# Performance work log

Measured on AMD Instinct MI355X. Metric: run time of the kernel, lower is better.

The kernel has to match this reference:

```python
import jax, jax.numpy as jnp
import numpy as np
from jax import lax

B, H, W, C, NH = 16, 64, 64, 192, 6


def rope2d(x, h, w, c, base=10000.0):
    # 2D RoPE: channel_dims=(h,w), k_max = c // 4; angles (h,w,c//2)
    kmax = c // 4
    theta = 1.0 / (base ** (jnp.arange(kmax, dtype=jnp.float32) / kmax))
    ai = jnp.broadcast_to(jnp.arange(h, dtype=jnp.float32)[:, None, None] * theta, (h, w, kmax))
    aj = jnp.broadcast_to(jnp.arange(w, dtype=jnp.float32)[None, :, None] * theta, (h, w, kmax))
    ang = jnp.concatenate([ai, aj], axis=-1)  # (h,w,c//2)
    cos, sin = jnp.cos(ang), jnp.sin(ang)
    xr = x.reshape(*x.shape[:-1], c // 2, 2)
    xe, xo = xr[..., 0], xr[..., 1]
    # complex multiply (cos + i sin) * (xe + i xo)
    return jnp.stack([xe * cos - xo * sin, xe * sin + xo * cos], axis=-1).reshape(x.shape)


def setup_inputs() -> dict:
    key = jax.random.key(0)
    ks = jax.random.split(key, 4)
    return {
        "x": jax.random.normal(ks[0], (B, H, W, C), dtype=jnp.float32),
        "qk_w": jax.random.normal(ks[1], (2 * C, C), dtype=jnp.float32) * 0.02,
        "qk_b": jnp.zeros((2 * C,), dtype=jnp.float32),
        "lepe_w": jax.random.normal(ks[2], (C, 1, 3, 3), dtype=jnp.float32) * 0.1,
        "lepe_b": jnp.zeros((C,), dtype=jnp.float32),
    }


def reference(x, qk_w, qk_b, lepe_w, lepe_b):
    b, h, w, c = x.shape
    n = h * w
    nh = NH
    d = c // nh
    qk = x @ qk_w.T + qk_b  # (b,h,w,2c)
    q = jax.nn.elu(qk[..., :c]) + 1.0
    k = jax.nn.elu(qk[..., c:]) + 1.0
    q_rope = rope2d(q, h, w, c).reshape(b, n, nh, d).transpose(0, 2, 1, 3)  # (b,nh,n,d)
    k_rope = rope2d(k, h, w, c).reshape(b, n, nh, d).transpose(0, 2, 1, 3)
    qh = q.reshape(b, n, nh, d).transpose(0, 2, 1, 3)
    kh = k.reshape(b, n, nh, d).transpose(0, 2, 1, 3)
    vh = x.reshape(b, n, nh, d).transpose(0, 2, 1, 3)  # v = x
    kmean = kh.mean(axis=2)  # (b,nh,d)
    z = 1.0 / (jnp.einsum('bhnd,bhd->bhn', qh, kmean)[..., None] + 1e-6)  # (b,nh,n,1)
    scale = 1.0 / jnp.sqrt(jnp.float32(n))
    kv = jnp.einsum('bhnd,bhne->bhde', k_rope * scale, vh * scale)  # (b,nh,d,d)
    out = jnp.einsum('bhnd,bhde->bhne', q_rope, kv) * z  # (b,nh,n,d)
    out = out.transpose(0, 2, 1, 3).reshape(b, n, c)
    # LePE: depthwise 3x3 conv on v (= x) in NCHW
    v_nchw = x.transpose(0, 3, 1, 2)
    lepe = lax.conv_general_dilated(v_nchw, lepe_w, (1, 1), 'SAME',
                                    dimension_numbers=('NCHW', 'OIHW', 'NCHW'),
                                    feature_group_count=c)
    lepe = lepe + lepe_b[None, :, None, None]
    return out + lepe.transpose(0, 2, 3, 1).reshape(b, n, c)
```

## Files before the change

kernel.cpp:

```cpp
#include <hip/hip_runtime.h>
#include <hip/hip_bf16.h>

using short8  = __attribute__((ext_vector_type(8))) short;
using floatx4 = __attribute__((ext_vector_type(4))) float;

#define CC 192
#define CN 4096
#define NHEAD 6
#define DHEAD 32
#define NZERO (16 * NHEAD * DHEAD * DHEAD + 16 * NHEAD * DHEAD)
#define ZBLK ((NZERO + 255) / 256)
#define TBLK ((CN * 96 + 255) / 256)

__device__ __forceinline__ float bf2f(short s) {
    return __uint_as_float(((unsigned)(unsigned short)s) << 16);
}
__device__ __forceinline__ short f2bf(float f) {
    __hip_bfloat16 h = __float2bfloat16(f);
    return *(short*)&h;
}

__global__ void k0_all(float* __restrict__ zp, unsigned* __restrict__ tabp,
                       const float* __restrict__ qkw, __hip_bfloat16* __restrict__ wfr)
{
    int bid = blockIdx.x;
    if (bid < ZBLK) {
        int i = bid * 256 + threadIdx.x;
        if (i < NZERO) zp[i] = 0.f;
    } else if (bid < ZBLK + TBLK) {
        int idx = (bid - ZBLK) * 256 + threadIdx.x;
        if (idx >= CN * 96) return;
        int n = idx / 96, c2 = idx - n * 96;
        int h = n >> 6, w = n & 63;
        int i = (c2 < 48) ? c2 : c2 - 48;
        float pos = (float)((c2 < 48) ? h : w);
        float theta = expf(-(float)i * (9.210340371976184f / 48.0f));
        float ang = pos * theta;
        unsigned c = (unsigned)(unsigned short)f2bf(cosf(ang));
        unsigned s = (unsigned)(unsigned short)f2bf(sinf(ang));
        tabp[idx] = c | (s << 16);
    } else {
        int tid = (bid - ZBLK - TBLK) * 256 + threadIdx.x;
        if (tid >= 24 * 6 * 64) return;
        int lane = tid & 63;
        int ks = (tid >> 6) % 6;
        int nig = tid / (6 * 64);
        int col = nig * 16 + (lane & 15);
        int k = ks * 32 + (lane >> 4) * 8;
        const float4* src = (const float4*)(qkw + (long)col * CC + k);
        float4 f0 = src[0], f1 = src[1];
        short8 s;
        s[0] = f2bf(f0.x); s[1] = f2bf(f0.y); s[2] = f2bf(f0.z); s[3] = f2bf(f0.w);
        s[4] = f2bf(f1.x); s[5] = f2bf(f1.y); s[6] = f2bf(f1.z); s[7] = f2bf(f1.w);
        *(short8*)&wfr[(long)tid * 8] = s;
    }
}

__global__ __launch_bounds__(512)
void k1_gemm(const float* __restrict__ x, const __hip_bfloat16* __restrict__ wfr,
             const float* __restrict__ qkb,
             __hip_bfloat16* __restrict__ qws, __hip_bfloat16* __restrict__ kws,
             __hip_bfloat16* __restrict__ xbf)
{
    __shared__ __align__(16) short A_lds[128 * 200];
    __shared__ __align__(16) short B_lds[24 * 512];

    const int tid  = threadIdx.x;
    const int wid  = tid >> 6, lane = tid & 63;
    const int wm   = wid >> 1, wn = wid & 1;
    const int lrow = lane & 15;
    const int l4   = lane >> 4;
    const long rowBase = (long)blockIdx.x * 128;

#pragma unroll
    for (int it = 0; it < 6; ++it) {
        int slot = it * 512 + tid;
        int row = slot / 24, c0 = (slot - (slot / 24) * 24) * 8;
        const float4* src = (const float4*)(x + (rowBase + row) * CC + c0);
        float4 f0 = src[0], f1 = src[1];
        short8 s;
        s[0] = f2bf(f0.x); s[1] = f2bf(f0.y); s[2] = f2bf(f0.z); s[3] = f2bf(f0.w);
        s[4] = f2bf(f1.x); s[5] = f2bf(f1.y); s[6] = f2bf(f1.z); s[7] = f2bf(f1.w);
        *(short8*)&A_lds[row * 200 + c0] = s;
        *(short8*)&xbf[(rowBase + row) * CC + c0] = s;
    }

    floatx4 acc[2][12];
#pragma unroll
    for (int i = 0; i < 2; ++i)
#pragma unroll
        for (int j = 0; j < 12; ++j) acc[i][j] = (floatx4)0.f;

    for (int ks = 0; ks < 6; ++ks) {
        short8 bst[3];
#pragma unroll
        for (int j = 0; j < 3; ++j) {
            int s = j * 512 + tid;
            bst[j] = *(const short8*)&wfr[((long)((s >> 6) * 6 + ks) * 64 + (s & 63)) * 8];
        }
        __syncthreads();
#pragma unroll
        for (int j = 0; j < 3; ++j) {
            int s = j * 512 + tid;
            *(short8*)&B_lds[s * 8] = bst[j];
        }
        __syncthreads();

        short8 a0 = *(const short8*)&A_lds[(wm * 32 + lrow) * 200 + ks * 32 + l4 * 8];
        short8 a1 = *(const short8*)&A_lds[(wm * 32 + 16 + lrow) * 200 + ks * 32 + l4 * 8];
#pragma unroll
        for (int ni = 0; ni < 12; ++ni) {
            short8 bf = *(const short8*)&B_lds[(wn * 12 + ni) * 512 + lane * 8];
            acc[0][ni] = __builtin_amdgcn_mfma_f32_16x16x32_bf16(a0, bf, acc[0][ni], 0, 0, 0);
            acc[1][ni] = __builtin_amdgcn_mfma_f32_16x16x32_bf16(a1, bf, acc[1][ni], 0, 0, 0);
        }
    }

    __hip_bfloat16* dstbase = wn ? kws : qws;
#pragma unroll
    for (int ni = 0; ni < 12; ++ni) {
        int col_l = ni * 16 + lrow;
        float bias = qkb[wn * 192 + col_l];
#pragma unroll
        for (int mi = 0; mi < 2; ++mi) {
#pragma unroll
            for (int r = 0; r < 4; ++r) {
                int rowl = wm * 32 + mi * 16 + l4 * 4 + r;
                long rowg = rowBase + rowl;
                float v = acc[mi][ni][r] + bias;
                v = (v > 0.f) ? (v + 1.f) : expf(v);
                dstbase[rowg * CC + col_l] = __float2bfloat16(v);
            }
        }
    }
}

__global__ __launch_bounds__(256)
void k2_kv(const __hip_bfloat16* __restrict__ kws, const __hip_bfloat16* __restrict__ xbf,
           const unsigned* __restrict__ tabp, float* __restrict__ kv, float* __restrict__ kmean)
{
    int bid = blockIdx.x;
    int chunk = bid & 7;
    int hd = (bid >> 3) % NHEAD;
    int b = bid / (8 * NHEAD);
    int tid = threadIdx.x;
    int lane = tid & 63;

    __shared__ __align__(16) float S[9248];
    float* kr_s = S;
    float* v_s  = S + 4608;
    float* km_s = S + 9216;

    if (tid < 32) km_s[tid] = 0.f;

    const int krow = tid >> 2, kq = tid & 3;
    const int rq = tid >> 6, tile = tid & 63;
    const int dq = tile >> 3, eq = tile & 7;

    float acc[4][4];
#pragma unroll
    for (int i = 0; i < 4; ++i)
#pragma unroll
        for (int j = 0; j < 4; ++j) acc[i][j] = 0.f;
    float msum[8];
#pragma unroll
    for (int j = 0; j < 8; ++j) msum[j] = 0.f;

    const int n0 = chunk * 512;
    const long rb = (long)b * CN;

    short8 k8[2], v8[2];
    uint4  u[2];
#pragma unroll
    for (int p = 0; p < 2; ++p) {
        int n = n0 + p * 64 + krow;
        k8[p] = *(const short8*)&kws[(rb + n) * CC + hd * DHEAD + kq * 8];
        v8[p] = *(const short8*)&xbf[(rb + n) * CC + hd * DHEAD + kq * 8];
        u[p]  = *(const uint4*)&tabp[(long)n * 96 + hd * 16 + kq * 4];
    }

    for (int batch = 0; batch < 4; ++batch) {
        if (batch) __syncthreads();
#pragma unroll
        for (int p = 0; p < 2; ++p) {
            int r = p * 64 + krow;
            float kf[8];
#pragma unroll
            for (int j = 0; j < 8; ++j) { kf[j] = bf2f(k8[p][j]); msum[j] += kf[j]; }
            float4 t0, t1;
            t0.x = bf2f((short)(u[p].x & 0xffff)); t0.y = bf2f((short)(u[p].x >> 16));
            t0.z = bf2f((short)(u[p].y & 0xffff)); t0.w = bf2f((short)(u[p].y >> 16));
            t1.x = bf2f((short)(u[p].z & 0xffff)); t1.y = bf2f((short)(u[p].z >> 16));
            t1.z = bf2f((short)(u[p].w & 0xffff)); t1.w = bf2f((short)(u[p].w >> 16));
            float4 r0, r1;
            r0.x = kf[0]*t0.x - kf[1]*t0.y;  r0.y = kf[0]*t0.y + kf[1]*t0.x;
            r0.z = kf[2]*t0.z - kf[3]*t0.w;  r0.w = kf[2]*t0.w + kf[3]*t0.z;
            r1.x = kf[4]*t1.x - kf[5]*t1.y;  r1.y = kf[4]*t1.y + kf[5]*t1.x;
            r1.z = kf[6]*t1.z - kf[7]*t1.w;  r1.w = kf[6]*t1.w + kf[7]*t1.z;
            *(float4*)&kr_s[r * 36 + kq * 8]     = r0;
            *(float4*)&kr_s[r * 36 + kq * 8 + 4] = r1;
            float4 va, vb;
            va.x = bf2f(v8[p][0]); va.y = bf2f(v8[p][1]); va.z = bf2f(v8[p][2]); va.w = bf2f(v8[p][3]);
            vb.x = bf2f(v8[p][4]); vb.y = bf2f(v8[p][5]); vb.z = bf2f(v8[p][6]); vb.w = bf2f(v8[p][7]);
            *(float4*)&v_s[r * 36 + kq * 8]     = va;
            *(float4*)&v_s[r * 36 + kq * 8 + 4] = vb;
        }
        if (batch < 3) {
#pragma unroll
            for (int p = 0; p < 2; ++p) {
                int n = n0 + (batch + 1) * 128 + p * 64 + krow;
                k8[p] = *(const short8*)&kws[(rb + n) * CC + hd * DHEAD + kq * 8];
                v8[p] = *(const short8*)&xbf[(rb + n) * CC + hd * DHEAD + kq * 8];
                u[p]  = *(const uint4*)&tabp[(long)n * 96 + hd * 16 + kq * 4];
            }
        }
        __syncthreads();
        const int rw = rq * 32;
#pragma unroll
        for (int rr = 0; rr < 32; ++rr) {
            int r = rw + rr;
            float4 k4 = *(const float4*)&kr_s[r * 36 + dq * 4];
            float4 v4 = *(const float4*)&v_s[r * 36 + eq * 4];
            acc[0][0] += k4.x * v4.x; acc[0][1] += k4.x * v4.y; acc[0][2] += k4.x * v4.z; acc[0][3] += k4.x * v4.w;
            acc[1][0] += k4.y * v4.x; acc[1][1] += k4.y * v4.y; acc[1][2] += k4.y * v4.z; acc[1][3] += k4.y * v4.w;
            acc[2][0] += k4.z * v4.x; acc[2][1] += k4.z * v4.y; acc[2][2] += k4.z * v4.z; acc[2][3] += k4.z * v4.w;
            acc[3][0] += k4.w * v4.x; acc[3][1] += k4.w * v4.y; acc[3][2] += k4.w * v4.z; acc[3][3] += k4.w * v4.w;
        }
    }
    __syncthreads();

    float* red = S;
#pragma unroll
    for (int i = 0; i < 4; ++i)
#pragma unroll
        for (int j = 0; j < 4; ++j)
            red[(i * 4 + j) * 256 + rq * 64 + tile] = acc[i][j];
#pragma unroll
    for (int j = 0; j < 8; ++j) {
        float m = msum[j];
        m += __shfl_down(m, 32);
        m += __shfl_down(m, 16);
        m += __shfl_down(m, 8);
        m += __shfl_down(m, 4);
        if (lane < 4) atomicAdd(&km_s[(tid & 3) * 8 + j], m);
    }
    __syncthreads();

    const float sc = 1.f / 4096.f;
    if (tid < 64) {
        float* kvb = kv + (long)(b * NHEAD + hd) * DHEAD * DHEAD;
#pragma unroll
        for (int i = 0; i < 4; ++i)
#pragma unroll
            for (int j = 0; j < 4; ++j) {
                int idx = (i * 4 + j) * 256 + tile;
                float s4 = red[idx] + red[idx + 64] + red[idx + 128] + red[idx + 192];
                atomicAdd(&kvb[(dq * 4 + i) * DHEAD + eq * 4 + j], s4 * sc);
            }
    }
    if (tid < 32) atomicAdd(&kmean[(b * NHEAD + hd) * DHEAD + tid], km_s[tid] * sc);
}

__global__ __launch_bounds__(256)
void k3_out(const __hip_bfloat16* __restrict__ qws, const __hip_bfloat16* __restrict__ xbf,
            const unsigned* __restrict__ tabp, const float* __restrict__ kv,
            const float* __restrict__ kmean, const float* __restrict__ lw,
            const float* __restrict__ lb, float* __restrict__ out)
{
    int raw = blockIdx.x;
    int bid = (raw & 7) * 128 + (raw >> 3);
    int b = bid >> 6, h = bid & 63;
    int tid = threadIdx.x;
    int wave = tid >> 6, lane = tid & 63, lrow = lane & 15, l4 = lane >> 4;

    __shared__ __align__(16) __hip_bfloat16 qa[64][104];
    __shared__ __align__(16) __hip_bfloat16 kvt[NHEAD][32][36];
    __shared__ __align__(16) float lwT[9][192];
    __shared__ float lb_lds[CC];
    __shared__ float km_lds[CC];
    __shared__ float zden[64][8];

    const long nbase = (long)b * CN + h * 64;

    const float* kvsrc = kv + (long)b * NHEAD * DHEAD * DHEAD;
    for (int i = tid; i < NHEAD * DHEAD * DHEAD; i += 256) {
        int hd = i >> 10, d = (i >> 5) & 31, e = i & 31;
        kvt[hd][e][d] = __float2bfloat16(kvsrc[i]);
    }
    if (tid < CC) { km_lds[tid] = kmean[b * CC + tid]; lb_lds[tid] = lb[tid]; }
    for (int i = tid; i < CC * 9; i += 256) {
        int c = i / 9, tap = i - c * 9;
        lwT[tap][c] = lw[i];
    }
    __syncthreads();

#pragma unroll
    for (int half = 0; half < 2; ++half) {
#pragma unroll
        for (int it = 0; it < 3; ++it) {
            int slot = it * 256 + tid;
            int w = slot / 12;
            int sub = slot - w * 12;
            int c0 = half * 96 + sub * 8;
            short8 qv = *(const short8*)&qws[(nbase + w) * CC + c0];
            float q[8];
#pragma unroll
            for (int j = 0; j < 8; ++j) q[j] = bf2f(qv[j]);
            float p = 0.f;
#pragma unroll
            for (int j = 0; j < 8; ++j) p += q[j] * km_lds[c0 + j];
            p += __shfl_xor(p, 1);
            p += __shfl_xor(p, 2);
            if ((sub & 3) == 0) zden[w][half * 3 + (sub >> 2)] = p;
            int n = h * 64 + w;
            uint4 u = *(const uint4*)&tabp[(long)n * 96 + (c0 >> 1)];
            float4 t0, t1;
            t0.x = bf2f((short)(u.x & 0xffff)); t0.y = bf2f((short)(u.x >> 16));
            t0.z = bf2f((short)(u.y & 0xffff)); t0.w = bf2f((short)(u.y >> 16));
            t1.x = bf2f((short)(u.z & 0xffff)); t1.y = bf2f((short)(u.z >> 16));
            t1.z = bf2f((short)(u.w & 0xffff)); t1.w = bf2f((short)(u.w >> 16));
            short8 qr;
            qr[0] = f2bf(q[0]*t0.x - q[1]*t0.y);  qr[1] = f2bf(q[0]*t0.y + q[1]*t0.x);
            qr[2] = f2bf(q[2]*t0.z - q[3]*t0.w);  qr[3] = f2bf(q[2]*t0.w + q[3]*t0.z);
            qr[4] = f2bf(q[4]*t1.x - q[5]*t1.y);  qr[5] = f2bf(q[4]*t1.y + q[5]*t1.x);
            qr[6] = f2bf(q[6]*t1.z - q[7]*t1.w);  qr[7] = f2bf(q[6]*t1.w + q[7]*t1.z);
            *(short8*)&qa[w][sub * 8] = qr;
        }
        __syncthreads();

        const int rt = wave;
        const int wbase = rt * 16 + l4 * 4;
#pragma unroll
        for (int hl = 0; hl < 3; ++hl) {
            int hd = half * 3 + hl;
            short8 a = *(const short8*)&qa[rt * 16 + lrow][hl * 32 + l4 * 8];
            float zv[4];
#pragma unroll
            for (int r = 0; r < 4; ++r) zv[r] = 1.f / (zden[wbase + r][hd] + 1e-6f);
#pragma unroll
            for (int nt = 0; nt < 2; ++nt) {
                short8 bfr = *(const short8*)&kvt[hd][nt * 16 + lrow][l4 * 8];
                floatx4 acc = __builtin_amdgcn_mfma_f32_16x16x32_bf16(a, bfr, (floatx4)0.f, 0, 0, 0);
                int col_l = hl * 32 + nt * 16 + lrow;
#pragma unroll
                for (int r = 0; r < 4; ++r)
                    qa[wbase + r][col_l] = __float2bfloat16(acc[r] * zv[r]);
            }
        }
        __syncthreads();

#pragma unroll
        for (int it = 0; it < 3; ++it) {
            int slot = it * 256 + tid;
            int w = slot / 12;
            int g = slot - w * 12;
            int c0g = g * 8;
            int c0 = half * 96 + c0g;
            float vals[8];
#pragma unroll
            for (int j = 0; j < 8; ++j) vals[j] = lb_lds[c0 + j];
#pragma unroll
            for (int dy = 0; dy < 3; ++dy) {
                int hy = h + dy - 1;
                if (hy < 0 || hy > 63) continue;
                const short* base = (const short*)xbf + (((long)b * 64 + hy) * 64) * CC + c0;
#pragma unroll
                for (int dx = 0; dx < 3; ++dx) {
                    int wx = w + dx - 1;
                    if (wx < 0 || wx > 63) continue;
                    short8 xv = *(const short8*)&base[(long)wx * CC];
                    const float4* wt4 = (const float4*)&lwT[dy * 3 + dx][c0];
                    float4 wa = wt4[0], wb = wt4[1];
                    vals[0] += bf2f(xv[0]) * wa.x;  vals[1] += bf2f(xv[1]) * wa.y;
                    vals[2] += bf2f(xv[2]) * wa.z;  vals[3] += bf2f(xv[3]) * wa.w;
                    vals[4] += bf2f(xv[4]) * wb.x;  vals[5] += bf2f(xv[5]) * wb.y;
                    vals[6] += bf2f(xv[6]) * wb.z;  vals[7] += bf2f(xv[7]) * wb.w;
                }
            }
            short8 at = *(const short8*)&qa[w][c0g];
#pragma unroll
            for (int j = 0; j < 8; ++j) vals[j] += bf2f(at[j]);
            float4 o0, o1;
            o0.x = vals[0]; o0.y = vals[1]; o0.z = vals[2]; o0.w = vals[3];
            o1.x = vals[4]; o1.y = vals[5]; o1.z = vals[6]; o1.w = vals[7];
            float* op = &out[(nbase + w) * CC + c0];
            *(float4*)op = o0;
            *(float4*)(op + 4) = o1;
        }
        __syncthreads();
    }
}

extern "C" void kernel_launch(void* const* d_in, const int* in_sizes, int n_in,
                              void* d_out, int out_size, void* d_ws, size_t ws_size,
                              hipStream_t stream)
{
    const float* x   = (const float*)d_in[0];
    const float* qkw = (const float*)d_in[1];
    const float* qkb = (const float*)d_in[2];
    const float* lw  = (const float*)d_in[3];
    const float* lb  = (const float*)d_in[4];
    float* out = (float*)d_out;

    char* ws = (char*)d_ws;
    unsigned* tabp = (unsigned*)ws;            ws += (size_t)CN * 96 * 4;
    __hip_bfloat16* qws = (__hip_bfloat16*)ws; ws += (size_t)16 * CN * CC * 2;
    __hip_bfloat16* kws = (__hip_bfloat16*)ws; ws += (size_t)16 * CN * CC * 2;
    __hip_bfloat16* xbf = (__hip_bfloat16*)ws; ws += (size_t)16 * CN * CC * 2;
    __hip_bfloat16* wfr = (__hip_bfloat16*)ws; ws += (size_t)24 * 6 * 64 * 8 * 2;
    float* kv = (float*)ws;                    ws += (size_t)16 * NHEAD * DHEAD * DHEAD * 4;
    float* km = (float*)ws;                    ws += (size_t)16 * NHEAD * DHEAD * 4;

    const int wblk = (24 * 6 * 64 + 255) / 256;
    k0_all<<<ZBLK + TBLK + wblk, 256, 0, stream>>>(kv, tabp, qkw, wfr);
    k1_gemm<<<512, 512, 0, stream>>>(x, wfr, qkb, qws, kws, xbf);
    k2_kv<<<16 * NHEAD * 8, 256, 0, stream>>>(kws, xbf, tabp, kv, km);
    k3_out<<<16 * 64, 256, 0, stream>>>(qws, xbf, tabp, kv, km, lw, lb, out);
}
```

Measured before the change: 103.9 us.

## Compute K^T V in k2_kv with bf16 MFMA 32x32x16 instead of scalar FMA

Replaces the scalar fp32 outer-product accumulation of rope(K)^T·V in the kv kernel with the bf16 MFMA 32x32x16 instruction. Rotated K and V are stored transposed in shared memory as bf16, with an XOR swizzle to avoid bank conflicts, and the cross-wave reduction is remapped to the MFMA output layout. This cuts VALU work and shared-memory footprint, but rounds the rotated K to bf16, which costs some precision.

```diff
diff --git a/kernel.cpp b/kernel.cpp
--- a/kernel.cpp
+++ b/kernel.cpp
@@ -1,8 +1,9 @@
 #include <hip/hip_runtime.h>
 #include <hip/hip_bf16.h>
 
-using short8  = __attribute__((ext_vector_type(8))) short;
-using floatx4 = __attribute__((ext_vector_type(4))) float;
+using short8   = __attribute__((ext_vector_type(8))) short;
+using floatx4  = __attribute__((ext_vector_type(4))) float;
+using floatx16 = __attribute__((ext_vector_type(16))) float;
 
 #define CC 192
 #define CN 4096
@@ -144,24 +145,18 @@
     int hd = (bid >> 3) % NHEAD;
     int b = bid / (8 * NHEAD);
     int tid = threadIdx.x;
-    int lane = tid & 63;
-
-    __shared__ __align__(16) float S[9248];
-    float* kr_s = S;
-    float* v_s  = S + 4608;
-    float* km_s = S + 9216;
+    int lane = tid & 63, wave = tid >> 6;
+
+    __shared__ __align__(16) short S[8192];
+    __shared__ float km_s[32];
+    char* krT = (char*)S;
+    char* vT  = (char*)S + 8192;
 
     if (tid < 32) km_s[tid] = 0.f;
 
     const int krow = tid >> 2, kq = tid & 3;
-    const int rq = tid >> 6, tile = tid & 63;
-    const int dq = tile >> 3, eq = tile & 7;
-
-    float acc[4][4];
-#pragma unroll
-    for (int i = 0; i < 4; ++i)
-#pragma unroll
-        for (int j = 0; j < 4; ++j) acc[i][j] = 0.f;
+
+    floatx16 acc = (floatx16)0.f;
     float msum[8];
 #pragma unroll
     for (int j = 0; j < 8; ++j) msum[j] = 0.f;
@@ -187,23 +182,24 @@
             float kf[8];
 #pragma unroll
             for (int j = 0; j < 8; ++j) { kf[j] = bf2f(k8[p][j]); msum[j] += kf[j]; }
-            float4 t0, t1;
-            t0.x = bf2f((short)(u[p].x & 0xffff)); t0.y = bf2f((short)(u[p].x >> 16));
-            t0.z = bf2f((short)(u[p].y & 0xffff)); t0.w = bf2f((short)(u[p].y >> 16));
-            t1.x = bf2f((short)(u[p].z & 0xffff)); t1.y = bf2f((short)(u[p].z >> 16));
-            t1.z = bf2f((short)(u[p].w & 0xffff)); t1.w = bf2f((short)(u[p].w >> 16));
-            float4 r0, r1;
-            r0.x = kf[0]*t0.x - kf[1]*t0.y;  r0.y = kf[0]*t0.y + kf[1]*t0.x;
-            r0.z = kf[2]*t0.z - kf[3]*t0.w;  r0.w = kf[2]*t0.w + kf[3]*t0.z;
-            r1.x = kf[4]*t1.x - kf[5]*t1.y;  r1.y = kf[4]*t1.y + kf[5]*t1.x;
-            r1.z = kf[6]*t1.z - kf[7]*t1.w;  r1.w = kf[6]*t1.w + kf[7]*t1.z;
-            *(float4*)&kr_s[r * 36 + kq * 8]     = r0;
-            *(float4*)&kr_s[r * 36 + kq * 8 + 4] = r1;
-            float4 va, vb;
-            va.x = bf2f(v8[p][0]); va.y = bf2f(v8[p][1]); va.z = bf2f(v8[p][2]); va.w = bf2f(v8[p][3]);
-            vb.x = bf2f(v8[p][4]); vb.y = bf2f(v8[p][5]); vb.z = bf2f(v8[p][6]); vb.w = bf2f(v8[p][7]);
-            *(float4*)&v_s[r * 36 + kq * 8]     = va;
-            *(float4*)&v_s[r * 36 + kq * 8 + 4] = vb;
+            float cs[4], sn[4];
+            cs[0] = bf2f((short)(u[p].x & 0xffff)); sn[0] = bf2f((short)(u[p].x >> 16));
+            cs[1] = bf2f((short)(u[p].y & 0xffff)); sn[1] = bf2f((short)(u[p].y >> 16));
+            cs[2] = bf2f((short)(u[p].z & 0xffff)); sn[2] = bf2f((short)(u[p].z >> 16));
+            cs[3] = bf2f((short)(u[p].w & 0xffff)); sn[3] = bf2f((short)(u[p].w >> 16));
+            short kr8[8];
+#pragma unroll
+            for (int q = 0; q < 4; ++q) {
+                kr8[2*q]   = f2bf(kf[2*q] * cs[q] - kf[2*q+1] * sn[q]);
+                kr8[2*q+1] = f2bf(kf[2*q] * sn[q] + kf[2*q+1] * cs[q]);
+            }
+#pragma unroll
+            for (int j = 0; j < 8; ++j) {
+                int ch = kq * 8 + j;
+                int byte = (ch * 256 + r * 2) ^ (j << 4);
+                *(short*)(krT + byte) = kr8[j];
+                *(short*)(vT  + byte) = v8[p][j];
+            }
         }
         if (batch < 3) {
 #pragma unroll
@@ -215,26 +211,23 @@
             }
         }
         __syncthreads();
-        const int rw = rq * 32;
-#pragma unroll
-        for (int rr = 0; rr < 32; ++rr) {
-            int r = rw + rr;
-            float4 k4 = *(const float4*)&kr_s[r * 36 + dq * 4];
-            float4 v4 = *(const float4*)&v_s[r * 36 + eq * 4];
-            acc[0][0] += k4.x * v4.x; acc[0][1] += k4.x * v4.y; acc[0][2] += k4.x * v4.z; acc[0][3] += k4.x * v4.w;
-            acc[1][0] += k4.y * v4.x; acc[1][1] += k4.y * v4.y; acc[1][2] += k4.y * v4.z; acc[1][3] += k4.y * v4.w;
-            acc[2][0] += k4.z * v4.x; acc[2][1] += k4.z * v4.y; acc[2][2] += k4.z * v4.z; acc[2][3] += k4.z * v4.w;
-            acc[3][0] += k4.w * v4.x; acc[3][1] += k4.w * v4.y; acc[3][2] += k4.w * v4.z; acc[3][3] += k4.w * v4.w;
+        const int d = lane & 31;
+        const int kh = (lane >> 5) * 8;
+#pragma unroll
+        for (int s = 0; s < 2; ++s) {
+            int k = wave * 32 + s * 16 + kh;
+            int abyte = (d * 256 + k * 2) ^ ((d & 7) << 4);
+            short8 af = *(const short8*)(krT + abyte);
+            short8 bf = *(const short8*)(vT + abyte);
+            acc = __builtin_amdgcn_mfma_f32_32x32x16_bf16(af, bf, acc, 0, 0, 0);
         }
     }
     __syncthreads();
 
-    float* red = S;
-#pragma unroll
-    for (int i = 0; i < 4; ++i)
-#pragma unroll
-        for (int j = 0; j < 4; ++j)
-            red[(i * 4 + j) * 256 + rq * 64 + tile] = acc[i][j];
+    float* red = (float*)S;
+#pragma unroll
+    for (int r = 0; r < 16; ++r)
+        red[(wave * 16 + r) * 64 + lane] = acc[r];
 #pragma unroll
     for (int j = 0; j < 8; ++j) {
         float m = msum[j];
@@ -247,16 +240,19 @@
     __syncthreads();
 
     const float sc = 1.f / 4096.f;
-    if (tid < 64) {
+    {
         float* kvb = kv + (long)(b * NHEAD + hd) * DHEAD * DHEAD;
-#pragma unroll
-        for (int i = 0; i < 4; ++i)
-#pragma unroll
-            for (int j = 0; j < 4; ++j) {
-                int idx = (i * 4 + j) * 256 + tile;
-                float s4 = red[idx] + red[idx + 64] + red[idx + 128] + red[idx + 192];
-                atomicAdd(&kvb[(dq * 4 + i) * DHEAD + eq * 4 + j], s4 * sc);
-            }
+        const int l = tid & 63;
+        const int rbase = (tid >> 6) * 4;
+#pragma unroll
+        for (int i = 0; i < 4; ++i) {
+            int r = rbase + i;
+            float v = red[(0 * 16 + r) * 64 + l] + red[(1 * 16 + r) * 64 + l]
+                    + red[(2 * 16 + r) * 64 + l] + red[(3 * 16 + r) * 64 + l];
+            int row = (r & 3) + 8 * (r >> 2) + 4 * (l >> 5);
+            int col = l & 31;
+            atomicAdd(&kvb[row * DHEAD + col], v * sc);
+        }
     }
     if (tid < 32) atomicAdd(&kmean[(b * NHEAD + hd) * DHEAD + tid], km_s[tid] * sc);
 }
```

New measurement: 91.49 us. 11.9% less time.
